# Kernel optimization log

Measured on AMD Instinct MI355X. Metric: run time of the kernel, lower is better.

## Reference

```python
import jax, jax.numpy as jnp
import numpy as np

TOP_K = 2


def setup_inputs() -> dict:
    key = jax.random.key(0)
    k1, k2, k3, k4 = jax.random.split(key, 4)
    B, S, D, F, E = 4, 2048, 1024, 4096, 8
    return {
        "inputs": jax.random.normal(k1, (B, S, D), dtype=jnp.float32),
        "gate_w": jax.random.normal(k2, (D, E), dtype=jnp.float32) * 0.02,
        "w1": jax.random.normal(k3, (E, D, F), dtype=jnp.float32) * 0.02,
        "w2": jax.random.normal(k4, (E, F, D), dtype=jnp.float32) * 0.02,
    }


def reference(inputs, gate_w, w1, w2):
    # gate logits: [B, S, E]
    gate_logits = jnp.einsum("bsd,de->bse", inputs, gate_w)
    E = gate_logits.shape[-1]

    # router KL loss (matches F.kl_div(log(mean_prob), uniform, reduction='batchmean')):
    # kl = sum(u * (log u - log p_mean)) / E   (batchmean divides by first dim = E)
    gate_prob = jax.nn.softmax(gate_logits.astype(jnp.float32), axis=-1).astype(inputs.dtype)
    mean_prob = gate_prob.mean(axis=(0, 1))  # [E]
    u = jnp.full((E,), 1.0 / E, dtype=mean_prob.dtype)
    kl_loss = jnp.sum(u * (jnp.log(u) - jnp.log(mean_prob))) / E

    # top-k routing
    weights, selected = jax.lax.top_k(gate_logits, TOP_K)  # [B,S,k]
    prob = jax.nn.softmax(weights.astype(jnp.float32), axis=-1).astype(inputs.dtype)

    # combine weight per expert: [B,S,E]; zero for unselected experts
    onehot = jax.nn.one_hot(selected, E, dtype=prob.dtype)  # [B,S,k,E]
    combine = jnp.einsum("bsk,bske->bse", prob, onehot)

    results = jnp.zeros_like(inputs)
    for i in range(E):  # fixed small loop over experts
        h = jax.nn.silu(jnp.einsum("bsd,df->bsf", inputs, w1[i]))
        out = jnp.einsum("bsf,fd->bsd", h, w2[i])
        results = results + combine[..., i : i + 1] * out
    return (results, kl_loss)
```

## Files before the change

kernel.cpp:

```cpp
#include <hip/hip_runtime.h>
#include <hip/hip_bf16.h>
#include <cstdint>


#define N_TOK 8192
#define D_DIM 1024
#define F_DIM 4096
#define N_EXP 8

#define CNT_OFF   0u
#define HOFF_OFF  32u
#define ZPG_OFF   128u
#define PSUM_OFF  256u
#define LIST_OFF  65792u
#define COEF_OFF  327936u
#define H1_OFF    1048576ull
#define XBF_OFF   1048576ull
#define W1T_OFF   18874368ull
#define W2T_OFF   (W1T_OFF + 67108864ull)
#define H2_OFF    (W2T_OFF + 67108864ull)
#define FULL_WS   (H2_OFF + 17408ull * 4096ull * 2ull)

typedef __attribute__((ext_vector_type(8))) short short8;
typedef __attribute__((ext_vector_type(4))) float f32x4;
typedef __attribute__((ext_vector_type(4))) float float4v;
typedef __attribute__((ext_vector_type(2))) unsigned int u32x2;

__device__ __forceinline__ unsigned short f2bf(float x) {
  unsigned int u = __float_as_uint(x);
  unsigned int r = (u + 0x7fffu + ((u >> 16) & 1u)) >> 16;
  return (unsigned short)r;
}

__device__ __forceinline__ void gload16(const void* g, void* l) {
  __builtin_amdgcn_global_load_lds(
      (const __attribute__((address_space(1))) void*)g,
      (__attribute__((address_space(3))) void*)l, 16, 0, 0);
}

__global__ void router_kernel(const float* __restrict__ x,
                              const float* __restrict__ gw,
                              int* __restrict__ cnt, int* __restrict__ list,
                              float* __restrict__ coef,
                              float* __restrict__ psum) {
  const int wave = threadIdx.x >> 6;
  const int lane = threadIdx.x & 63;
  const int t = blockIdx.x * 4 + wave;

  __shared__ float bps[N_EXP];
  if (threadIdx.x < N_EXP) bps[threadIdx.x] = 0.f;
  __syncthreads();

  float lg[8] = {0.f, 0.f, 0.f, 0.f, 0.f, 0.f, 0.f, 0.f};
  const float* xr = x + (size_t)t * D_DIM;
#pragma unroll
  for (int i = 0; i < 16; ++i) {
    int d = lane + i * 64;
    float xv = xr[d];
    float4v w0 = *(const float4v*)(gw + d * 8);
    float4v w1 = *(const float4v*)(gw + d * 8 + 4);
    lg[0] = fmaf(xv, w0.x, lg[0]); lg[1] = fmaf(xv, w0.y, lg[1]);
    lg[2] = fmaf(xv, w0.z, lg[2]); lg[3] = fmaf(xv, w0.w, lg[3]);
    lg[4] = fmaf(xv, w1.x, lg[4]); lg[5] = fmaf(xv, w1.y, lg[5]);
    lg[6] = fmaf(xv, w1.z, lg[6]); lg[7] = fmaf(xv, w1.w, lg[7]);
  }
#pragma unroll
  for (int m = 32; m; m >>= 1) {
#pragma unroll
    for (int e = 0; e < 8; ++e) lg[e] += __shfl_xor(lg[e], m);
  }

  if (lane == 0) {
    float mx = lg[0];
#pragma unroll
    for (int e = 1; e < 8; ++e) mx = fmaxf(mx, lg[e]);
    float p[8], s = 0.f;
#pragma unroll
    for (int e = 0; e < 8; ++e) { p[e] = expf(lg[e] - mx); s += p[e]; }
    float inv = 1.f / s;
#pragma unroll
    for (int e = 0; e < 8; ++e) atomicAdd(&bps[e], p[e] * inv);

    int i0 = 0;
#pragma unroll
    for (int e = 1; e < 8; ++e) if (lg[e] > lg[i0]) i0 = e;
    int i1 = (i0 == 0) ? 1 : 0;
#pragma unroll
    for (int e = 0; e < 8; ++e) if (e != i1 && e != i0 && lg[e] > lg[i1]) i1 = e;
    float p0 = 1.f / (1.f + expf(lg[i1] - lg[i0]));
    float p1 = 1.f - p0;
    int s0 = atomicAdd(&cnt[i0], 1);
    list[i0 * N_TOK + s0] = t; coef[i0 * N_TOK + s0] = p0;
    int s1 = atomicAdd(&cnt[i1], 1);
    list[i1 * N_TOK + s1] = t; coef[i1 * N_TOK + s1] = p1;
  }
  __syncthreads();
  if (threadIdx.x < 8) psum[blockIdx.x * 8 + threadIdx.x] = bps[threadIdx.x];
}

__global__ void prefix_kernel(const int* __restrict__ cnt, int* __restrict__ hoff) {
  if (threadIdx.x == 0) {
    int o = 0;
#pragma unroll
    for (int e = 0; e < 8; ++e) {
      hoff[e] = o;
      o += ((cnt[e] + 127) >> 7) << 7;
    }
    hoff[8] = o;
  }
}

__global__ void kl_kernel(const float* __restrict__ psum, float* __restrict__ out_kl) {
  __shared__ float s[8];
  if (threadIdx.x < 8) s[threadIdx.x] = 0.f;
  __syncthreads();
  float loc[8] = {0.f, 0.f, 0.f, 0.f, 0.f, 0.f, 0.f, 0.f};
  for (int r = threadIdx.x; r < 2048; r += 256) {
#pragma unroll
    for (int e = 0; e < 8; ++e) loc[e] += psum[r * 8 + e];
  }
#pragma unroll
  for (int e = 0; e < 8; ++e) atomicAdd(&s[e], loc[e]);
  __syncthreads();
  if (threadIdx.x == 0) {
    float kl = 0.f;
#pragma unroll
    for (int e = 0; e < 8; ++e) {
      float mean = s[e] / 8192.f;
      kl += (logf(0.125f) - logf(mean));
    }
    out_kl[0] = kl * (0.125f * 0.125f);
  }
}

__global__ void xconv_kernel(const float* __restrict__ x,
                             unsigned short* __restrict__ xbf) {
  size_t i = ((size_t)blockIdx.x * 256 + threadIdx.x) * 8;
  float4v a = *(const float4v*)(x + i);
  float4v b = *(const float4v*)(x + i + 4);
  short8 o;
  o[0] = (short)f2bf(a.x); o[1] = (short)f2bf(a.y);
  o[2] = (short)f2bf(a.z); o[3] = (short)f2bf(a.w);
  o[4] = (short)f2bf(b.x); o[5] = (short)f2bf(b.y);
  o[6] = (short)f2bf(b.z); o[7] = (short)f2bf(b.w);
  *(short8*)(xbf + i) = o;
}

__global__ __launch_bounds__(256) void wtrans_kernel(
    const float* __restrict__ w, unsigned short* __restrict__ wt, int K, int N) {
  const int e = blockIdx.z;
  const int n0 = blockIdx.x * 64, k0 = blockIdx.y * 64;
  __shared__ float t[64][65];
  const float* we = w + (size_t)e * K * N;
  const int nl = threadIdx.x & 63;
  const int kl4 = threadIdx.x >> 6;
#pragma unroll
  for (int r = 0; r < 16; ++r) {
    int kl = r * 4 + kl4;
    t[kl][nl] = we[(size_t)(k0 + kl) * N + n0 + nl];
  }
  __syncthreads();
  unsigned short* wte = wt + (size_t)e * K * N;
  const int kp = (threadIdx.x & 31) * 2;
  const int nl8 = threadIdx.x >> 5;
#pragma unroll
  for (int r = 0; r < 8; ++r) {
    int n = r * 8 + nl8;
    unsigned int pk = (unsigned int)f2bf(t[kp][n]) |
                      ((unsigned int)f2bf(t[kp + 1][n]) << 16);
    *(unsigned int*)(wte + (size_t)(n0 + n) * K + k0 + kp) = pk;
  }
}

__device__ __forceinline__ short8 ld_frag(const unsigned short* base, int row_base,
                                          int k_base, int lane) {
  int row = row_base + (lane & 15);
  int byte = (row * 128 + (k_base + ((lane >> 4) << 3)) * 2) ^ ((row & 7) << 4);
  return *(const short8*)((const char*)base + byte);
}

__global__ __launch_bounds__(256) void gemm1_v2(
    const unsigned short* __restrict__ xbf, const unsigned short* __restrict__ w1t,
    const int* __restrict__ cnt, const int* __restrict__ hoff,
    const int* __restrict__ list, const unsigned short* __restrict__ zpage,
    unsigned short* __restrict__ h) {
  const int e = blockIdx.z, mblk = blockIdx.y, nblk = blockIdx.x;
  const int c = cnt[e];
  if (mblk * 128 >= c) return;
  const int tid = threadIdx.x, lane = tid & 63, wave = tid >> 6;
  const int wm = (wave >> 1) * 64, wn = (wave & 1) * 64;

  __shared__ unsigned short At[128 * 64];
  __shared__ unsigned short Bt[128 * 64];

  const int wb = (tid * 16) & 127;
  const int rowb = tid >> 3;
  const int sw = wb ^ ((rowb & 7) << 4);
  const char* asrc[4]; int astep[4];
  const char* bsrc[4];
#pragma unroll
  for (int i = 0; i < 4; ++i) {
    int row = i * 32 + rowb;
    int slot = mblk * 128 + row;
    if (slot < c) {
      int tok = list[e * N_TOK + slot];
      asrc[i] = (const char*)(xbf + (size_t)tok * D_DIM) + sw;
      astep[i] = 128;
    } else {
      asrc[i] = (const char*)zpage + sw;
      astep[i] = 0;
    }
    bsrc[i] = (const char*)(w1t + ((size_t)e * F_DIM + nblk * 128 + row) * D_DIM) + sw;
  }

  f32x4 acc[4][4];
#pragma unroll
  for (int i = 0; i < 4; ++i)
#pragma unroll
    for (int j = 0; j < 4; ++j) acc[i][j] = f32x4{0.f, 0.f, 0.f, 0.f};

  char* ldsA = (char*)At;
  char* ldsB = (char*)Bt;
  for (int kc = 0; kc < 16; ++kc) {
    __syncthreads();
#pragma unroll
    for (int i = 0; i < 4; ++i) {
      gload16(asrc[i], ldsA + i * 4096 + wave * 1024);
      gload16(bsrc[i], ldsB + i * 4096 + wave * 1024);
      asrc[i] += astep[i];
      bsrc[i] += 128;
    }
    __syncthreads();
#pragma unroll
    for (int ks = 0; ks < 2; ++ks) {
      short8 af[4], bb[4];
#pragma unroll
      for (int mf = 0; mf < 4; ++mf) af[mf] = ld_frag(At, wm + mf * 16, ks * 32, lane);
#pragma unroll
      for (int nf = 0; nf < 4; ++nf) bb[nf] = ld_frag(Bt, wn + nf * 16, ks * 32, lane);
#pragma unroll
      for (int mf = 0; mf < 4; ++mf)
#pragma unroll
        for (int nf = 0; nf < 4; ++nf)
          acc[mf][nf] = __builtin_amdgcn_mfma_f32_16x16x32_bf16(
              af[mf], bb[nf], acc[mf][nf], 0, 0, 0);
    }
  }

  const int hbase = hoff[e] + mblk * 128;
#pragma unroll
  for (int mf = 0; mf < 4; ++mf)
#pragma unroll
    for (int nf = 0; nf < 4; ++nf)
#pragma unroll
      for (int r = 0; r < 4; ++r) {
        float v = acc[mf][nf][r];
        v = v / (1.f + __expf(-v));
        int row = wm + mf * 16 + ((lane >> 4) << 2) + r;
        int col = nblk * 128 + wn + nf * 16 + (lane & 15);
        h[(size_t)(hbase + row) * F_DIM + col] = f2bf(v);
      }
}

__global__ __launch_bounds__(256) void gemm2_v2(
    const unsigned short* __restrict__ h, const unsigned short* __restrict__ w2t,
    const int* __restrict__ cnt, const int* __restrict__ hoff,
    const int* __restrict__ list, const float* __restrict__ coef,
    float* __restrict__ out) {
  const int e = blockIdx.z, mblk = blockIdx.y, nblk = blockIdx.x;
  const int c = cnt[e];
  if (mblk * 128 >= c) return;
  const int tid = threadIdx.x, lane = tid & 63, wave = tid >> 6;
  const int wm = (wave >> 1) * 64, wn = (wave & 1) * 64;

  __shared__ unsigned short At[128 * 64];
  __shared__ unsigned short Bt[128 * 64];

  const int wb = (tid * 16) & 127;
  const int rowb = tid >> 3;
  const int sw = wb ^ ((rowb & 7) << 4);
  const int hbase = hoff[e] + mblk * 128;
  const char* asrc[4];
  const char* bsrc[4];
#pragma unroll
  for (int i = 0; i < 4; ++i) {
    int row = i * 32 + rowb;
    asrc[i] = (const char*)(h + (size_t)(hbase + row) * F_DIM) + sw;
    bsrc[i] = (const char*)(w2t + ((size_t)e * D_DIM + nblk * 128 + row) * F_DIM) + sw;
  }

  f32x4 acc[4][4];
#pragma unroll
  for (int i = 0; i < 4; ++i)
#pragma unroll
    for (int j = 0; j < 4; ++j) acc[i][j] = f32x4{0.f, 0.f, 0.f, 0.f};

  char* ldsA = (char*)At;
  char* ldsB = (char*)Bt;
  for (int kc = 0; kc < 64; ++kc) {
    __syncthreads();
#pragma unroll
    for (int i = 0; i < 4; ++i) {
      gload16(asrc[i], ldsA + i * 4096 + wave * 1024);
      gload16(bsrc[i], ldsB + i * 4096 + wave * 1024);
      asrc[i] += 128;
      bsrc[i] += 128;
    }
    __syncthreads();
#pragma unroll
    for (int ks = 0; ks < 2; ++ks) {
      short8 af[4], bb[4];
#pragma unroll
      for (int mf = 0; mf < 4; ++mf) af[mf] = ld_frag(At, wm + mf * 16, ks * 32, lane);
#pragma unroll
      for (int nf = 0; nf < 4; ++nf) bb[nf] = ld_frag(Bt, wn + nf * 16, ks * 32, lane);
#pragma unroll
      for (int mf = 0; mf < 4; ++mf)
#pragma unroll
        for (int nf = 0; nf < 4; ++nf)
          acc[mf][nf] = __builtin_amdgcn_mfma_f32_16x16x32_bf16(
              af[mf], bb[nf], acc[mf][nf], 0, 0, 0);
    }
  }

#pragma unroll
  for (int mf = 0; mf < 4; ++mf) {
#pragma unroll
    for (int r = 0; r < 4; ++r) {
      int slot = mblk * 128 + wm + mf * 16 + ((lane >> 4) << 2) + r;
      if (slot < c) {
        int tok = list[e * N_TOK + slot];
        float cf = coef[e * N_TOK + slot];
#pragma unroll
        for (int nf = 0; nf < 4; ++nf) {
          int col = nblk * 128 + wn + nf * 16 + (lane & 15);
          unsafeAtomicAdd(&out[(size_t)tok * D_DIM + col], cf * acc[mf][nf][r]);
        }
      }
    }
  }
}

__global__ __launch_bounds__(256) void gemm1_v1(
    const float* __restrict__ x, const float* __restrict__ w1,
    const int* __restrict__ cnt, const int* __restrict__ hoff,
    const int* __restrict__ list, unsigned short* __restrict__ h) {
  const int e = blockIdx.z, mblk = blockIdx.y, nblk = blockIdx.x;
  const int c = cnt[e];
  if (mblk * 128 >= c) return;
  const int tid = threadIdx.x, lane = tid & 63, wave = tid >> 6;
  const int wm = (wave >> 1) * 64, wn = (wave & 1) * 64;

  __shared__ unsigned short At[128 * 64];
  __shared__ unsigned short Bt[128 * 64];
  __shared__ int toks[128];
  if (tid < 128) {
    int slot = mblk * 128 + tid;
    toks[tid] = (slot < c) ? list[e * N_TOK + slot] : -1;
  }
  __syncthreads();

  f32x4 acc[4][4];
#pragma unroll
  for (int i = 0; i < 4; ++i)
#pragma unroll
    for (int j = 0; j < 4; ++j) acc[i][j] = f32x4{0.f, 0.f, 0.f, 0.f};

  const float* w1e = w1 + (size_t)e * D_DIM * F_DIM;
  for (int kc = 0; kc < 16; ++kc) {
    __syncthreads();
#pragma unroll
    for (int it = 0; it < 8; ++it) {
      int lin = it * 256 + tid;
      int row = lin >> 4, c4 = lin & 15;
      int tok = toks[row];
      unsigned int lo = 0u, hi = 0u;
      if (tok >= 0) {
        float4v f = *(const float4v*)(x + (size_t)tok * D_DIM + kc * 64 + c4 * 4);
        lo = (unsigned int)f2bf(f.x) | ((unsigned int)f2bf(f.y) << 16);
        hi = (unsigned int)f2bf(f.z) | ((unsigned int)f2bf(f.w) << 16);
      }
      int byte = (row * 128 + c4 * 8) ^ ((row & 7) << 4);
      *(u32x2*)((char*)At + byte) = u32x2{lo, hi};
    }
#pragma unroll
    for (int it = 0; it < 16; ++it) {
      int lin = it * 256 + tid;
      int f_loc = lin & 127, dp = lin >> 7;
      int d = kc * 64 + dp * 2;
      const float* src = w1e + (size_t)d * F_DIM + nblk * 128 + f_loc;
      unsigned int pk = (unsigned int)f2bf(src[0]) |
                        ((unsigned int)f2bf(src[F_DIM]) << 16);
      int byte = (f_loc * 128 + dp * 4) ^ ((f_loc & 7) << 4);
      *(unsigned int*)((char*)Bt + byte) = pk;
    }
    __syncthreads();
#pragma unroll
    for (int ks = 0; ks < 2; ++ks) {
      short8 af[4], bb[4];
#pragma unroll
      for (int mf = 0; mf < 4; ++mf) af[mf] = ld_frag(At, wm + mf * 16, ks * 32, lane);
#pragma unroll
      for (int nf = 0; nf < 4; ++nf) bb[nf] = ld_frag(Bt, wn + nf * 16, ks * 32, lane);
#pragma unroll
      for (int mf = 0; mf < 4; ++mf)
#pragma unroll
        for (int nf = 0; nf < 4; ++nf)
          acc[mf][nf] = __builtin_amdgcn_mfma_f32_16x16x32_bf16(
              af[mf], bb[nf], acc[mf][nf], 0, 0, 0);
    }
  }

  const int hbase = hoff[e] + mblk * 128;
#pragma unroll
  for (int mf = 0; mf < 4; ++mf)
#pragma unroll
    for (int nf = 0; nf < 4; ++nf)
#pragma unroll
      for (int r = 0; r < 4; ++r) {
        float v = acc[mf][nf][r];
        v = v / (1.f + __expf(-v));
        int row = wm + mf * 16 + ((lane >> 4) << 2) + r;
        int col = nblk * 128 + wn + nf * 16 + (lane & 15);
        h[(size_t)(hbase + row) * F_DIM + col] = f2bf(v);
      }
}

__global__ __launch_bounds__(256) void gemm2_v1(
    const unsigned short* __restrict__ h, const float* __restrict__ w2,
    const int* __restrict__ cnt, const int* __restrict__ hoff,
    const int* __restrict__ list, const float* __restrict__ coef,
    float* __restrict__ out) {
  const int e = blockIdx.z, mblk = blockIdx.y, nblk = blockIdx.x;
  const int c = cnt[e];
  if (mblk * 128 >= c) return;
  const int tid = threadIdx.x, lane = tid & 63, wave = tid >> 6;
  const int wm = (wave >> 1) * 64, wn = (wave & 1) * 64;

  __shared__ unsigned short At[128 * 64];
  __shared__ unsigned short Bt[128 * 64];

  f32x4 acc[4][4];
#pragma unroll
  for (int i = 0; i < 4; ++i)
#pragma unroll
    for (int j = 0; j < 4; ++j) acc[i][j] = f32x4{0.f, 0.f, 0.f, 0.f};

  const int hbase = hoff[e] + mblk * 128;
  const float* w2e = w2 + (size_t)e * F_DIM * D_DIM;
  for (int kc = 0; kc < 64; ++kc) {
    __syncthreads();
#pragma unroll
    for (int it = 0; it < 8; ++it) {
      int lin = it * 256 + tid;
      int row = lin >> 4, c4 = lin & 15;
      u32x2 v = *(const u32x2*)(h + (size_t)(hbase + row) * F_DIM + kc * 64 + c4 * 4);
      int byte = (row * 128 + c4 * 8) ^ ((row & 7) << 4);
      *(u32x2*)((char*)At + byte) = v;
    }
#pragma unroll
    for (int it = 0; it < 16; ++it) {
      int lin = it * 256 + tid;
      int dcol = lin & 127, kp = lin >> 7;
      int k = kc * 64 + kp * 2;
      const float* src = w2e + (size_t)k * D_DIM + nblk * 128 + dcol;
      unsigned int pk = (unsigned int)f2bf(src[0]) |
                        ((unsigned int)f2bf(src[D_DIM]) << 16);
      int byte = (dcol * 128 + kp * 4) ^ ((dcol & 7) << 4);
      *(unsigned int*)((char*)Bt + byte) = pk;
    }
    __syncthreads();
#pragma unroll
    for (int ks = 0; ks < 2; ++ks) {
      short8 af[4], bb[4];
#pragma unroll
      for (int mf = 0; mf < 4; ++mf) af[mf] = ld_frag(At, wm + mf * 16, ks * 32, lane);
#pragma unroll
      for (int nf = 0; nf < 4; ++nf) bb[nf] = ld_frag(Bt, wn + nf * 16, ks * 32, lane);
#pragma unroll
      for (int mf = 0; mf < 4; ++mf)
#pragma unroll
        for (int nf = 0; nf < 4; ++nf)
          acc[mf][nf] = __builtin_amdgcn_mfma_f32_16x16x32_bf16(
              af[mf], bb[nf], acc[mf][nf], 0, 0, 0);
    }
  }

#pragma unroll
  for (int mf = 0; mf < 4; ++mf) {
#pragma unroll
    for (int r = 0; r < 4; ++r) {
      int slot = mblk * 128 + wm + mf * 16 + ((lane >> 4) << 2) + r;
      if (slot < c) {
        int tok = list[e * N_TOK + slot];
        float cf = coef[e * N_TOK + slot];
#pragma unroll
        for (int nf = 0; nf < 4; ++nf) {
          int col = nblk * 128 + wn + nf * 16 + (lane & 15);
          unsafeAtomicAdd(&out[(size_t)tok * D_DIM + col], cf * acc[mf][nf][r]);
        }
      }
    }
  }
}

extern "C" void kernel_launch(void* const* d_in, const int* in_sizes, int n_in,
                              void* d_out, int out_size, void* d_ws, size_t ws_size,
                              hipStream_t stream) {
  const float* x = (const float*)d_in[0];
  const float* gw = (const float*)d_in[1];
  const float* w1 = (const float*)d_in[2];
  const float* w2 = (const float*)d_in[3];
  float* out = (float*)d_out;
  char* ws = (char*)d_ws;

  int* cnt = (int*)(ws + CNT_OFF);
  int* hoff = (int*)(ws + HOFF_OFF);
  float* psum = (float*)(ws + PSUM_OFF);
  int* list = (int*)(ws + LIST_OFF);
  float* coef = (float*)(ws + COEF_OFF);

  hipMemsetAsync(d_ws, 0, PSUM_OFF + 2048 * 8 * 4, stream);
  hipMemsetAsync(d_out, 0, (size_t)out_size * 4, stream);

  router_kernel<<<2048, 256, 0, stream>>>(x, gw, cnt, list, coef, psum);
  prefix_kernel<<<1, 64, 0, stream>>>(cnt, hoff);
  kl_kernel<<<1, 256, 0, stream>>>(psum, out + 8388608);

  if (ws_size >= FULL_WS) {
    unsigned short* xbf = (unsigned short*)(ws + XBF_OFF);
    unsigned short* w1t = (unsigned short*)(ws + W1T_OFF);
    unsigned short* w2t = (unsigned short*)(ws + W2T_OFF);
    unsigned short* h = (unsigned short*)(ws + H2_OFF);
    const unsigned short* zpage = (const unsigned short*)(ws + ZPG_OFF);

    xconv_kernel<<<4096, 256, 0, stream>>>(x, xbf);
    wtrans_kernel<<<dim3(64, 16, 8), 256, 0, stream>>>(w1, w1t, 1024, 4096);
    wtrans_kernel<<<dim3(16, 64, 8), 256, 0, stream>>>(w2, w2t, 4096, 1024);
    gemm1_v2<<<dim3(32, 64, 8), 256, 0, stream>>>(xbf, w1t, cnt, hoff, list, zpage, h);
    gemm2_v2<<<dim3(8, 64, 8), 256, 0, stream>>>(h, w2t, cnt, hoff, list, coef, out);
  } else {
    unsigned short* h = (unsigned short*)(ws + H1_OFF);
    gemm1_v1<<<dim3(32, 64, 8), 256, 0, stream>>>(x, w1, cnt, hoff, list, h);
    gemm2_v1<<<dim3(8, 64, 8), 256, 0, stream>>>(h, w2, cnt, hoff, list, coef, out);
  }
}
```

Measured before the change: 845.5 us.

## Enlarge expert GEMM tiles to 256x256 with double-buffered LDS and fuse bf16 conversion

```diff
diff --git a/kernel.cpp b/kernel.cpp
--- a/kernel.cpp
+++ b/kernel.cpp
@@ -19,7 +19,7 @@
 #define W1T_OFF   18874368ull
 #define W2T_OFF   (W1T_OFF + 67108864ull)
 #define H2_OFF    (W2T_OFF + 67108864ull)
-#define FULL_WS   (H2_OFF + 17408ull * 4096ull * 2ull)
+#define FULL_WS   (H2_OFF + 18432ull * 4096ull * 2ull)
 
 typedef __attribute__((ext_vector_type(8))) short short8;
 typedef __attribute__((ext_vector_type(4))) float f32x4;
@@ -42,7 +42,8 @@
                               const float* __restrict__ gw,
                               int* __restrict__ cnt, int* __restrict__ list,
                               float* __restrict__ coef,
-                              float* __restrict__ psum) {
+                              float* __restrict__ psum,
+                              unsigned short* __restrict__ xbf) {
   const int wave = threadIdx.x >> 6;
   const int lane = threadIdx.x & 63;
   const int t = blockIdx.x * 4 + wave;
@@ -53,10 +54,12 @@
 
   float lg[8] = {0.f, 0.f, 0.f, 0.f, 0.f, 0.f, 0.f, 0.f};
   const float* xr = x + (size_t)t * D_DIM;
+  unsigned short* xbr = xbf + (size_t)t * D_DIM;
 #pragma unroll
   for (int i = 0; i < 16; ++i) {
     int d = lane + i * 64;
     float xv = xr[d];
+    xbr[d] = f2bf(xv);
     float4v w0 = *(const float4v*)(gw + d * 8);
     float4v w1 = *(const float4v*)(gw + d * 8 + 4);
     lg[0] = fmaf(xv, w0.x, lg[0]); lg[1] = fmaf(xv, w0.y, lg[1]);
@@ -98,13 +101,14 @@
   if (threadIdx.x < 8) psum[blockIdx.x * 8 + threadIdx.x] = bps[threadIdx.x];
 }
 
-__global__ void prefix_kernel(const int* __restrict__ cnt, int* __restrict__ hoff) {
+__global__ void prefix_kernel(const int* __restrict__ cnt, int* __restrict__ hoff,
+                              int g) {
   if (threadIdx.x == 0) {
     int o = 0;
 #pragma unroll
     for (int e = 0; e < 8; ++e) {
       hoff[e] = o;
-      o += ((cnt[e] + 127) >> 7) << 7;
+      o += (cnt[e] + g - 1) & ~(g - 1);
     }
     hoff[8] = o;
   }
@@ -131,19 +135,6 @@
     }
     out_kl[0] = kl * (0.125f * 0.125f);
   }
-}
-
-__global__ void xconv_kernel(const float* __restrict__ x,
-                             unsigned short* __restrict__ xbf) {
-  size_t i = ((size_t)blockIdx.x * 256 + threadIdx.x) * 8;
-  float4v a = *(const float4v*)(x + i);
-  float4v b = *(const float4v*)(x + i + 4);
-  short8 o;
-  o[0] = (short)f2bf(a.x); o[1] = (short)f2bf(a.y);
-  o[2] = (short)f2bf(a.z); o[3] = (short)f2bf(a.w);
-  o[4] = (short)f2bf(b.x); o[5] = (short)f2bf(b.y);
-  o[6] = (short)f2bf(b.z); o[7] = (short)f2bf(b.w);
-  *(short8*)(xbf + i) = o;
 }
 
 __global__ __launch_bounds__(256) void wtrans_kernel(
@@ -179,29 +170,40 @@
   return *(const short8*)((const char*)base + byte);
 }
 
-__global__ __launch_bounds__(256) void gemm1_v2(
+#define STAGE_TILE(buf)                                                    \
+  {                                                                        \
+    char* la_ = (char*)As + (buf) * 32768 + wave * 1024;                   \
+    char* lb_ = (char*)Bs + (buf) * 32768 + wave * 1024;                   \
+    _Pragma("unroll") for (int i_ = 0; i_ < 4; ++i_) {                     \
+      gload16(asrc[i_], la_ + i_ * 8192);                                  \
+      gload16(bsrc[i_], lb_ + i_ * 8192);                                  \
+      asrc[i_] += astep[i_];                                               \
+      bsrc[i_] += 128;                                                     \
+    }                                                                      \
+  }
+
+__global__ __launch_bounds__(512, 2) void gemm1_v3(
     const unsigned short* __restrict__ xbf, const unsigned short* __restrict__ w1t,
     const int* __restrict__ cnt, const int* __restrict__ hoff,
     const int* __restrict__ list, const unsigned short* __restrict__ zpage,
     unsigned short* __restrict__ h) {
   const int e = blockIdx.z, mblk = blockIdx.y, nblk = blockIdx.x;
   const int c = cnt[e];
-  if (mblk * 128 >= c) return;
+  if (mblk * 256 >= c) return;
   const int tid = threadIdx.x, lane = tid & 63, wave = tid >> 6;
-  const int wm = (wave >> 1) * 64, wn = (wave & 1) * 64;
-
-  __shared__ unsigned short At[128 * 64];
-  __shared__ unsigned short Bt[128 * 64];
-
-  const int wb = (tid * 16) & 127;
-  const int rowb = tid >> 3;
-  const int sw = wb ^ ((rowb & 7) << 4);
+  const int wm = wave >> 2, wn = wave & 3;
+
+  __shared__ unsigned short As[2][16384];
+  __shared__ unsigned short Bs[2][16384];
+
+  const int rowb = wave * 8 + (lane >> 3);
+  const int sw = ((lane & 7) ^ (lane >> 3)) << 4;
   const char* asrc[4]; int astep[4];
   const char* bsrc[4];
 #pragma unroll
   for (int i = 0; i < 4; ++i) {
-    int row = i * 32 + rowb;
-    int slot = mblk * 128 + row;
+    int row = i * 64 + rowb;
+    int slot = mblk * 256 + row;
     if (slot < c) {
       int tok = list[e * N_TOK + slot];
       asrc[i] = (const char*)(xbf + (size_t)tok * D_DIM) + sw;
@@ -210,130 +212,124 @@
       asrc[i] = (const char*)zpage + sw;
       astep[i] = 0;
     }
-    bsrc[i] = (const char*)(w1t + ((size_t)e * F_DIM + nblk * 128 + row) * D_DIM) + sw;
-  }
-
-  f32x4 acc[4][4];
-#pragma unroll
-  for (int i = 0; i < 4; ++i)
+    bsrc[i] = (const char*)(w1t + ((size_t)e * F_DIM + nblk * 256 + row) * D_DIM) + sw;
+  }
+
+  f32x4 acc[8][4];
+#pragma unroll
+  for (int i = 0; i < 8; ++i)
 #pragma unroll
     for (int j = 0; j < 4; ++j) acc[i][j] = f32x4{0.f, 0.f, 0.f, 0.f};
 
-  char* ldsA = (char*)At;
-  char* ldsB = (char*)Bt;
+  STAGE_TILE(0);
+  __syncthreads();
+  int cur = 0;
   for (int kc = 0; kc < 16; ++kc) {
-    __syncthreads();
-#pragma unroll
-    for (int i = 0; i < 4; ++i) {
-      gload16(asrc[i], ldsA + i * 4096 + wave * 1024);
-      gload16(bsrc[i], ldsB + i * 4096 + wave * 1024);
-      asrc[i] += astep[i];
-      bsrc[i] += 128;
-    }
-    __syncthreads();
+    if (kc + 1 < 16) STAGE_TILE(cur ^ 1);
+    const unsigned short* At = As[cur];
+    const unsigned short* Bt = Bs[cur];
 #pragma unroll
     for (int ks = 0; ks < 2; ++ks) {
-      short8 af[4], bb[4];
-#pragma unroll
-      for (int mf = 0; mf < 4; ++mf) af[mf] = ld_frag(At, wm + mf * 16, ks * 32, lane);
-#pragma unroll
-      for (int nf = 0; nf < 4; ++nf) bb[nf] = ld_frag(Bt, wn + nf * 16, ks * 32, lane);
-#pragma unroll
-      for (int mf = 0; mf < 4; ++mf)
+      short8 a[8], b[4];
+#pragma unroll
+      for (int mf = 0; mf < 8; ++mf) a[mf] = ld_frag(At, wm * 128 + mf * 16, ks * 32, lane);
+#pragma unroll
+      for (int nf = 0; nf < 4; ++nf) b[nf] = ld_frag(Bt, wn * 64 + nf * 16, ks * 32, lane);
+#pragma unroll
+      for (int mf = 0; mf < 8; ++mf)
 #pragma unroll
         for (int nf = 0; nf < 4; ++nf)
           acc[mf][nf] = __builtin_amdgcn_mfma_f32_16x16x32_bf16(
-              af[mf], bb[nf], acc[mf][nf], 0, 0, 0);
-    }
-  }
-
-  const int hbase = hoff[e] + mblk * 128;
-#pragma unroll
-  for (int mf = 0; mf < 4; ++mf)
+              a[mf], b[nf], acc[mf][nf], 0, 0, 0);
+    }
+    __syncthreads();
+    cur ^= 1;
+  }
+
+  const int hbase = hoff[e] + mblk * 256;
+#pragma unroll
+  for (int mf = 0; mf < 8; ++mf)
 #pragma unroll
     for (int nf = 0; nf < 4; ++nf)
 #pragma unroll
       for (int r = 0; r < 4; ++r) {
         float v = acc[mf][nf][r];
         v = v / (1.f + __expf(-v));
-        int row = wm + mf * 16 + ((lane >> 4) << 2) + r;
-        int col = nblk * 128 + wn + nf * 16 + (lane & 15);
+        int row = wm * 128 + mf * 16 + ((lane >> 4) << 2) + r;
+        int col = nblk * 256 + wn * 64 + nf * 16 + (lane & 15);
         h[(size_t)(hbase + row) * F_DIM + col] = f2bf(v);
       }
 }
 
-__global__ __launch_bounds__(256) void gemm2_v2(
+__global__ __launch_bounds__(512, 2) void gemm2_v3(
     const unsigned short* __restrict__ h, const unsigned short* __restrict__ w2t,
     const int* __restrict__ cnt, const int* __restrict__ hoff,
     const int* __restrict__ list, const float* __restrict__ coef,
     float* __restrict__ out) {
   const int e = blockIdx.z, mblk = blockIdx.y, nblk = blockIdx.x;
   const int c = cnt[e];
-  if (mblk * 128 >= c) return;
+  if (mblk * 256 >= c) return;
   const int tid = threadIdx.x, lane = tid & 63, wave = tid >> 6;
-  const int wm = (wave >> 1) * 64, wn = (wave & 1) * 64;
-
-  __shared__ unsigned short At[128 * 64];
-  __shared__ unsigned short Bt[128 * 64];
-
-  const int wb = (tid * 16) & 127;
-  const int rowb = tid >> 3;
-  const int sw = wb ^ ((rowb & 7) << 4);
-  const int hbase = hoff[e] + mblk * 128;
-  const char* asrc[4];
+  const int wm = wave >> 2, wn = wave & 3;
+
+  __shared__ unsigned short As[2][16384];
+  __shared__ unsigned short Bs[2][16384];
+
+  const int rowb = wave * 8 + (lane >> 3);
+  const int sw = ((lane & 7) ^ (lane >> 3)) << 4;
+  const int hbase = hoff[e] + mblk * 256;
+  const char* asrc[4]; int astep[4];
   const char* bsrc[4];
 #pragma unroll
   for (int i = 0; i < 4; ++i) {
-    int row = i * 32 + rowb;
+    int row = i * 64 + rowb;
     asrc[i] = (const char*)(h + (size_t)(hbase + row) * F_DIM) + sw;
-    bsrc[i] = (const char*)(w2t + ((size_t)e * D_DIM + nblk * 128 + row) * F_DIM) + sw;
-  }
-
-  f32x4 acc[4][4];
-#pragma unroll
-  for (int i = 0; i < 4; ++i)
+    astep[i] = 128;
+    bsrc[i] = (const char*)(w2t + ((size_t)e * D_DIM + nblk * 256 + row) * F_DIM) + sw;
+  }
+
+  f32x4 acc[8][4];
+#pragma unroll
+  for (int i = 0; i < 8; ++i)
 #pragma unroll
     for (int j = 0; j < 4; ++j) acc[i][j] = f32x4{0.f, 0.f, 0.f, 0.f};
 
-  char* ldsA = (char*)At;
-  char* ldsB = (char*)Bt;
+  STAGE_TILE(0);
+  __syncthreads();
+  int cur = 0;
   for (int kc = 0; kc < 64; ++kc) {
-    __syncthreads();
-#pragma unroll
-    for (int i = 0; i < 4; ++i) {
-      gload16(asrc[i], ldsA + i * 4096 + wave * 1024);
-      gload16(bsrc[i], ldsB + i * 4096 + wave * 1024);
-      asrc[i] += 128;
-      bsrc[i] += 128;
-    }
-    __syncthreads();
+    if (kc + 1 < 64) STAGE_TILE(cur ^ 1);
+    const unsigned short* At = As[cur];
+    const unsigned short* Bt = Bs[cur];
 #pragma unroll
     for (int ks = 0; ks < 2; ++ks) {
-      short8 af[4], bb[4];
-#pragma unroll
-      for (int mf = 0; mf < 4; ++mf) af[mf] = ld_frag(At, wm + mf * 16, ks * 32, lane);
-#pragma unroll
-      for (int nf = 0; nf < 4; ++nf) bb[nf] = ld_frag(Bt, wn + nf * 16, ks * 32, lane);
-#pragma unroll
-      for (int mf = 0; mf < 4; ++mf)
+      short8 a[8], b[4];
+#pragma unroll
+      for (int mf = 0; mf < 8; ++mf) a[mf] = ld_frag(At, wm * 128 + mf * 16, ks * 32, lane);
+#pragma unroll
+      for (int nf = 0; nf < 4; ++nf) b[nf] = ld_frag(Bt, wn * 64 + nf * 16, ks * 32, lane);
+#pragma unroll
+      for (int mf = 0; mf < 8; ++mf)
 #pragma unroll
         for (int nf = 0; nf < 4; ++nf)
           acc[mf][nf] = __builtin_amdgcn_mfma_f32_16x16x32_bf16(
-              af[mf], bb[nf], acc[mf][nf], 0, 0, 0);
-    }
-  }
-
-#pragma unroll
-  for (int mf = 0; mf < 4; ++mf) {
+              a[mf], b[nf], acc[mf][nf], 0, 0, 0);
+    }
+    __syncthreads();
+    cur ^= 1;
+  }
+
+#pragma unroll
+  for (int mf = 0; mf < 8; ++mf) {
 #pragma unroll
     for (int r = 0; r < 4; ++r) {
-      int slot = mblk * 128 + wm + mf * 16 + ((lane >> 4) << 2) + r;
+      int slot = mblk * 256 + wm * 128 + mf * 16 + ((lane >> 4) << 2) + r;
       if (slot < c) {
         int tok = list[e * N_TOK + slot];
         float cf = coef[e * N_TOK + slot];
 #pragma unroll
         for (int nf = 0; nf < 4; ++nf) {
-          int col = nblk * 128 + wn + nf * 16 + (lane & 15);
+          int col = nblk * 256 + wn * 64 + nf * 16 + (lane & 15);
           unsafeAtomicAdd(&out[(size_t)tok * D_DIM + col], cf * acc[mf][nf][r]);
         }
       }
@@ -519,26 +515,27 @@
   float* psum = (float*)(ws + PSUM_OFF);
   int* list = (int*)(ws + LIST_OFF);
   float* coef = (float*)(ws + COEF_OFF);
+  unsigned short* xbf = (unsigned short*)(ws + XBF_OFF);
+
+  const bool full = (ws_size >= FULL_WS);
 
   hipMemsetAsync(d_ws, 0, PSUM_OFF + 2048 * 8 * 4, stream);
   hipMemsetAsync(d_out, 0, (size_t)out_size * 4, stream);
 
-  router_kernel<<<2048, 256, 0, stream>>>(x, gw, cnt, list, coef, psum);
-  prefix_kernel<<<1, 64, 0, stream>>>(cnt, hoff);
+  router_kernel<<<2048, 256, 0, stream>>>(x, gw, cnt, list, coef, psum, xbf);
+  prefix_kernel<<<1, 64, 0, stream>>>(cnt, hoff, full ? 256 : 128);
   kl_kernel<<<1, 256, 0, stream>>>(psum, out + 8388608);
 
-  if (ws_size >= FULL_WS) {
-    unsigned short* xbf = (unsigned short*)(ws + XBF_OFF);
+  if (full) {
     unsigned short* w1t = (unsigned short*)(ws + W1T_OFF);
     unsigned short* w2t = (unsigned short*)(ws + W2T_OFF);
     unsigned short* h = (unsigned short*)(ws + H2_OFF);
     const unsigned short* zpage = (const unsigned short*)(ws + ZPG_OFF);
 
-    xconv_kernel<<<4096, 256, 0, stream>>>(x, xbf);
     wtrans_kernel<<<dim3(64, 16, 8), 256, 0, stream>>>(w1, w1t, 1024, 4096);
     wtrans_kernel<<<dim3(16, 64, 8), 256, 0, stream>>>(w2, w2t, 4096, 1024);
-    gemm1_v2<<<dim3(32, 64, 8), 256, 0, stream>>>(xbf, w1t, cnt, hoff, list, zpage, h);
-    gemm2_v2<<<dim3(8, 64, 8), 256, 0, stream>>>(h, w2t, cnt, hoff, list, coef, out);
+    gemm1_v3<<<dim3(16, 32, 8), 512, 0, stream>>>(xbf, w1t, cnt, hoff, list, zpage, h);
+    gemm2_v3<<<dim3(4, 32, 8), 512, 0, stream>>>(h, w2t, cnt, hoff, list, coef, out);
   } else {
     unsigned short* h = (unsigned short*)(ws + H1_OFF);
     gemm1_v1<<<dim3(32, 64, 8), 256, 0, stream>>>(x, w1, cnt, hoff, list, h);
```

After: 863.3 us. 1.02x slower.

## Double-buffer LDS in expert GEMMs, compact grid via block map, fuse bf16 convert

Applied to the files above, without the earlier changes.

```diff
diff --git a/kernel.cpp b/kernel.cpp
--- a/kernel.cpp
+++ b/kernel.cpp
@@ -7,13 +7,17 @@
 #define D_DIM 1024
 #define F_DIM 4096
 #define N_EXP 8
+#define MB_MAX 136
 
 #define CNT_OFF   0u
-#define HOFF_OFF  32u
+#define HOFF_OFF  64u
+#define NMB_OFF   104u
 #define ZPG_OFF   128u
-#define PSUM_OFF  256u
-#define LIST_OFF  65792u
-#define COEF_OFF  327936u
+#define MBE_OFF   256u
+#define MBB_OFF   896u
+#define PSUM_OFF  1536u
+#define LIST_OFF  67072u
+#define COEF_OFF  329216u
 #define H1_OFF    1048576ull
 #define XBF_OFF   1048576ull
 #define W1T_OFF   18874368ull
@@ -42,7 +46,8 @@
                               const float* __restrict__ gw,
                               int* __restrict__ cnt, int* __restrict__ list,
                               float* __restrict__ coef,
-                              float* __restrict__ psum) {
+                              float* __restrict__ psum,
+                              unsigned short* __restrict__ xbf) {
   const int wave = threadIdx.x >> 6;
   const int lane = threadIdx.x & 63;
   const int t = blockIdx.x * 4 + wave;
@@ -53,10 +58,12 @@
 
   float lg[8] = {0.f, 0.f, 0.f, 0.f, 0.f, 0.f, 0.f, 0.f};
   const float* xr = x + (size_t)t * D_DIM;
+  unsigned short* xbr = xbf + (size_t)t * D_DIM;
 #pragma unroll
   for (int i = 0; i < 16; ++i) {
     int d = lane + i * 64;
     float xv = xr[d];
+    xbr[d] = f2bf(xv);
     float4v w0 = *(const float4v*)(gw + d * 8);
     float4v w1 = *(const float4v*)(gw + d * 8 + 4);
     lg[0] = fmaf(xv, w0.x, lg[0]); lg[1] = fmaf(xv, w0.y, lg[1]);
@@ -98,15 +105,19 @@
   if (threadIdx.x < 8) psum[blockIdx.x * 8 + threadIdx.x] = bps[threadIdx.x];
 }
 
-__global__ void prefix_kernel(const int* __restrict__ cnt, int* __restrict__ hoff) {
+__global__ void prefix_kernel(const int* __restrict__ cnt, int* __restrict__ hoff,
+                              int* __restrict__ mbe, int* __restrict__ mbb,
+                              int* __restrict__ nmb, int g) {
   if (threadIdx.x == 0) {
-    int o = 0;
-#pragma unroll
+    int o = 0, gmb = 0;
     for (int e = 0; e < 8; ++e) {
       hoff[e] = o;
-      o += ((cnt[e] + 127) >> 7) << 7;
+      int nb = (cnt[e] + g - 1) / g;
+      for (int m = 0; m < nb; ++m) { mbe[gmb] = e; mbb[gmb] = m; ++gmb; }
+      o += nb * g;
     }
     hoff[8] = o;
+    *nmb = gmb;
   }
 }
 
@@ -131,19 +142,6 @@
     }
     out_kl[0] = kl * (0.125f * 0.125f);
   }
-}
-
-__global__ void xconv_kernel(const float* __restrict__ x,
-                             unsigned short* __restrict__ xbf) {
-  size_t i = ((size_t)blockIdx.x * 256 + threadIdx.x) * 8;
-  float4v a = *(const float4v*)(x + i);
-  float4v b = *(const float4v*)(x + i + 4);
-  short8 o;
-  o[0] = (short)f2bf(a.x); o[1] = (short)f2bf(a.y);
-  o[2] = (short)f2bf(a.z); o[3] = (short)f2bf(a.w);
-  o[4] = (short)f2bf(b.x); o[5] = (short)f2bf(b.y);
-  o[6] = (short)f2bf(b.z); o[7] = (short)f2bf(b.w);
-  *(short8*)(xbf + i) = o;
 }
 
 __global__ __launch_bounds__(256) void wtrans_kernel(
@@ -179,23 +177,37 @@
   return *(const short8*)((const char*)base + byte);
 }
 
-__global__ __launch_bounds__(256) void gemm1_v2(
+#define STAGE4(buf)                                                        \
+  {                                                                        \
+    char* la_ = (char*)As + (buf) * 16384 + wave * 1024;                   \
+    char* lb_ = (char*)Bs + (buf) * 16384 + wave * 1024;                   \
+    _Pragma("unroll") for (int i_ = 0; i_ < 4; ++i_) {                     \
+      gload16(asrc[i_], la_ + i_ * 4096);                                  \
+      gload16(bsrc[i_], lb_ + i_ * 4096);                                  \
+      asrc[i_] += astep[i_];                                               \
+      bsrc[i_] += 128;                                                     \
+    }                                                                      \
+  }
+
+__global__ __launch_bounds__(256, 2) void gemm1_v4(
     const unsigned short* __restrict__ xbf, const unsigned short* __restrict__ w1t,
     const int* __restrict__ cnt, const int* __restrict__ hoff,
+    const int* __restrict__ mbe, const int* __restrict__ mbb,
+    const int* __restrict__ nmb,
     const int* __restrict__ list, const unsigned short* __restrict__ zpage,
     unsigned short* __restrict__ h) {
-  const int e = blockIdx.z, mblk = blockIdx.y, nblk = blockIdx.x;
+  const int mb = blockIdx.y;
+  if (mb >= *nmb) return;
+  const int e = mbe[mb], mblk = mbb[mb], nblk = blockIdx.x;
   const int c = cnt[e];
-  if (mblk * 128 >= c) return;
   const int tid = threadIdx.x, lane = tid & 63, wave = tid >> 6;
   const int wm = (wave >> 1) * 64, wn = (wave & 1) * 64;
 
-  __shared__ unsigned short At[128 * 64];
-  __shared__ unsigned short Bt[128 * 64];
-
-  const int wb = (tid * 16) & 127;
+  __shared__ unsigned short As[2][8192];
+  __shared__ unsigned short Bs[2][8192];
+
   const int rowb = tid >> 3;
-  const int sw = wb ^ ((rowb & 7) << 4);
+  const int sw = (((tid & 7) ^ (rowb & 7)) << 4);
   const char* asrc[4]; int astep[4];
   const char* bsrc[4];
 #pragma unroll
@@ -219,18 +231,13 @@
 #pragma unroll
     for (int j = 0; j < 4; ++j) acc[i][j] = f32x4{0.f, 0.f, 0.f, 0.f};
 
-  char* ldsA = (char*)At;
-  char* ldsB = (char*)Bt;
+  STAGE4(0);
+  __syncthreads();
+  int cur = 0;
   for (int kc = 0; kc < 16; ++kc) {
-    __syncthreads();
-#pragma unroll
-    for (int i = 0; i < 4; ++i) {
-      gload16(asrc[i], ldsA + i * 4096 + wave * 1024);
-      gload16(bsrc[i], ldsB + i * 4096 + wave * 1024);
-      asrc[i] += astep[i];
-      bsrc[i] += 128;
-    }
-    __syncthreads();
+    if (kc + 1 < 16) STAGE4(cur ^ 1);
+    const unsigned short* At = As[cur];
+    const unsigned short* Bt = Bs[cur];
 #pragma unroll
     for (int ks = 0; ks < 2; ++ks) {
       short8 af[4], bb[4];
@@ -245,6 +252,8 @@
           acc[mf][nf] = __builtin_amdgcn_mfma_f32_16x16x32_bf16(
               af[mf], bb[nf], acc[mf][nf], 0, 0, 0);
     }
+    __syncthreads();
+    cur ^= 1;
   }
 
   const int hbase = hoff[e] + mblk * 128;
@@ -262,30 +271,33 @@
       }
 }
 
-__global__ __launch_bounds__(256) void gemm2_v2(
+__global__ __launch_bounds__(256, 2) void gemm2_v4(
     const unsigned short* __restrict__ h, const unsigned short* __restrict__ w2t,
     const int* __restrict__ cnt, const int* __restrict__ hoff,
+    const int* __restrict__ mbe, const int* __restrict__ mbb,
+    const int* __restrict__ nmb,
     const int* __restrict__ list, const float* __restrict__ coef,
     float* __restrict__ out) {
-  const int e = blockIdx.z, mblk = blockIdx.y, nblk = blockIdx.x;
+  const int mb = blockIdx.y;
+  if (mb >= *nmb) return;
+  const int e = mbe[mb], mblk = mbb[mb], nblk = blockIdx.x;
   const int c = cnt[e];
-  if (mblk * 128 >= c) return;
   const int tid = threadIdx.x, lane = tid & 63, wave = tid >> 6;
   const int wm = (wave >> 1) * 64, wn = (wave & 1) * 64;
 
-  __shared__ unsigned short At[128 * 64];
-  __shared__ unsigned short Bt[128 * 64];
-
-  const int wb = (tid * 16) & 127;
+  __shared__ unsigned short As[2][8192];
+  __shared__ unsigned short Bs[2][8192];
+
   const int rowb = tid >> 3;
-  const int sw = wb ^ ((rowb & 7) << 4);
+  const int sw = (((tid & 7) ^ (rowb & 7)) << 4);
   const int hbase = hoff[e] + mblk * 128;
-  const char* asrc[4];
+  const char* asrc[4]; int astep[4];
   const char* bsrc[4];
 #pragma unroll
   for (int i = 0; i < 4; ++i) {
     int row = i * 32 + rowb;
     asrc[i] = (const char*)(h + (size_t)(hbase + row) * F_DIM) + sw;
+    astep[i] = 128;
     bsrc[i] = (const char*)(w2t + ((size_t)e * D_DIM + nblk * 128 + row) * F_DIM) + sw;
   }
 
@@ -295,18 +307,13 @@
 #pragma unroll
     for (int j = 0; j < 4; ++j) acc[i][j] = f32x4{0.f, 0.f, 0.f, 0.f};
 
-  char* ldsA = (char*)At;
-  char* ldsB = (char*)Bt;
+  STAGE4(0);
+  __syncthreads();
+  int cur = 0;
   for (int kc = 0; kc < 64; ++kc) {
-    __syncthreads();
-#pragma unroll
-    for (int i = 0; i < 4; ++i) {
-      gload16(asrc[i], ldsA + i * 4096 + wave * 1024);
-      gload16(bsrc[i], ldsB + i * 4096 + wave * 1024);
-      asrc[i] += 128;
-      bsrc[i] += 128;
-    }
-    __syncthreads();
+    if (kc + 1 < 64) STAGE4(cur ^ 1);
+    const unsigned short* At = As[cur];
+    const unsigned short* Bt = Bs[cur];
 #pragma unroll
     for (int ks = 0; ks < 2; ++ks) {
       short8 af[4], bb[4];
@@ -321,6 +328,8 @@
           acc[mf][nf] = __builtin_amdgcn_mfma_f32_16x16x32_bf16(
               af[mf], bb[nf], acc[mf][nf], 0, 0, 0);
     }
+    __syncthreads();
+    cur ^= 1;
   }
 
 #pragma unroll
@@ -516,29 +525,33 @@
 
   int* cnt = (int*)(ws + CNT_OFF);
   int* hoff = (int*)(ws + HOFF_OFF);
+  int* nmb = (int*)(ws + NMB_OFF);
+  int* mbe = (int*)(ws + MBE_OFF);
+  int* mbb = (int*)(ws + MBB_OFF);
   float* psum = (float*)(ws + PSUM_OFF);
   int* list = (int*)(ws + LIST_OFF);
   float* coef = (float*)(ws + COEF_OFF);
+  unsigned short* xbf = (unsigned short*)(ws + XBF_OFF);
 
   hipMemsetAsync(d_ws, 0, PSUM_OFF + 2048 * 8 * 4, stream);
   hipMemsetAsync(d_out, 0, (size_t)out_size * 4, stream);
 
-  router_kernel<<<2048, 256, 0, stream>>>(x, gw, cnt, list, coef, psum);
-  prefix_kernel<<<1, 64, 0, stream>>>(cnt, hoff);
+  router_kernel<<<2048, 256, 0, stream>>>(x, gw, cnt, list, coef, psum, xbf);
+  prefix_kernel<<<1, 64, 0, stream>>>(cnt, hoff, mbe, mbb, nmb, 128);
   kl_kernel<<<1, 256, 0, stream>>>(psum, out + 8388608);
 
   if (ws_size >= FULL_WS) {
-    unsigned short* xbf = (unsigned short*)(ws + XBF_OFF);
     unsigned short* w1t = (unsigned short*)(ws + W1T_OFF);
     unsigned short* w2t = (unsigned short*)(ws + W2T_OFF);
     unsigned short* h = (unsigned short*)(ws + H2_OFF);
     const unsigned short* zpage = (const unsigned short*)(ws + ZPG_OFF);
 
-    xconv_kernel<<<4096, 256, 0, stream>>>(x, xbf);
     wtrans_kernel<<<dim3(64, 16, 8), 256, 0, stream>>>(w1, w1t, 1024, 4096);
     wtrans_kernel<<<dim3(16, 64, 8), 256, 0, stream>>>(w2, w2t, 4096, 1024);
-    gemm1_v2<<<dim3(32, 64, 8), 256, 0, stream>>>(xbf, w1t, cnt, hoff, list, zpage, h);
-    gemm2_v2<<<dim3(8, 64, 8), 256, 0, stream>>>(h, w2t, cnt, hoff, list, coef, out);
+    gemm1_v4<<<dim3(32, MB_MAX), 256, 0, stream>>>(xbf, w1t, cnt, hoff, mbe, mbb,
+                                                   nmb, list, zpage, h);
+    gemm2_v4<<<dim3(8, MB_MAX), 256, 0, stream>>>(h, w2t, cnt, hoff, mbe, mbb,
+                                                  nmb, list, coef, out);
   } else {
     unsigned short* h = (unsigned short*)(ws + H1_OFF);
     gemm1_v1<<<dim3(32, 64, 8), 256, 0, stream>>>(x, w1, cnt, hoff, list, h);
```

Measured after the change: 956.7 us. 13.2% more time.
